# Optimization experiments

Hardware: AMD Instinct MI355X
Metric: run time of the kernel (lower is better)

The kernel has to match this reference:

```python
import jax, jax.numpy as jnp
import numpy as np

DIM = 1024
NUM_HEADS = 16
HEAD_DIM = DIM // NUM_HEADS


def setup_inputs() -> dict:
    key = jax.random.key(0)
    k1, k2, k3, k4, k5 = jax.random.split(key, 5)
    B, N, C = 4, 4096, DIM
    s = 1.0 / np.sqrt(C)
    return {
        "x": jax.random.normal(k1, (B, N, C), dtype=jnp.float32),
        "W_qkv": jax.random.uniform(k2, (C, 3 * C), dtype=jnp.float32, minval=-s, maxval=s),
        "b_qkv": jax.random.uniform(k3, (3 * C,), dtype=jnp.float32, minval=-s, maxval=s),
        "W_proj": jax.random.uniform(k4, (C, C), dtype=jnp.float32, minval=-s, maxval=s),
        "b_proj": jax.random.uniform(k5, (C,), dtype=jnp.float32, minval=-s, maxval=s),
    }


def reference(x, W_qkv, b_qkv, W_proj, b_proj):
    B, N, C = x.shape
    H, D = NUM_HEADS, HEAD_DIM
    qkv = x @ W_qkv + b_qkv                      # [B,N,3C]
    qkv = qkv.reshape(B, N, 3, H, D).transpose(2, 0, 3, 1, 4)  # [3,B,H,N,D]
    q, k, v = qkv[0], qkv[1], qkv[2]
    q = jax.nn.softmax(q, axis=-1)               # softmax over head_dim
    k = jax.nn.softmax(k, axis=-2)               # softmax over sequence N
    context = jnp.einsum('bhnd,bhne->bhde', k, v)  # [B,H,D,D]
    out = jnp.einsum('bhnd,bhde->bhne', q, context)  # [B,H,N,D]
    out = out.transpose(0, 2, 1, 3).reshape(B, N, C)
    return out @ W_proj + b_proj
```

## Files before the change

### kernel.cpp

```cpp
#include <hip/hip_runtime.h>

#define BBATCH 4
#define SEQ 4096
#define CC 1024
#define HH 16
#define DD 64
#define TOKENS 16384
#define QKV3 3072

typedef __attribute__((ext_vector_type(8))) short short8;
typedef __attribute__((ext_vector_type(4))) float floatx4;

__device__ __forceinline__ unsigned short f2bf(float x) {
    unsigned int u = __float_as_uint(x);
    u += 0x7fff + ((u >> 16) & 1);
    return (unsigned short)(u >> 16);
}
__device__ __forceinline__ float bf2f(unsigned short h) {
    return __uint_as_float((unsigned int)h << 16);
}

__device__ __forceinline__ void gload_lds16(const void* g, void* l) {
    __builtin_amdgcn_global_load_lds(
        (const __attribute__((address_space(1))) unsigned int*)g,
        (__attribute__((address_space(3))) unsigned int*)l, 16, 0, 0);
}

__global__ __launch_bounds__(256) void cvt_bf16_kernel(
    const float* __restrict__ X, unsigned short* __restrict__ Y, long n4)
{
    long i = (long)blockIdx.x * 256 + threadIdx.x;
    if (i >= n4) return;
    float4 v = *reinterpret_cast<const float4*>(&X[i * 4]);
    ushort4 h;
    h.x = f2bf(v.x); h.y = f2bf(v.y); h.z = f2bf(v.z); h.w = f2bf(v.w);
    *reinterpret_cast<ushort4*>(&Y[i * 4]) = h;
}

__global__ __launch_bounds__(256) void transpose_bf16_kernel(
    const float* __restrict__ W, int K, int N, unsigned short* __restrict__ T)
{
    __shared__ unsigned short Lh[32][36];
    const int k0 = blockIdx.y * 32, n0 = blockIdx.x * 32;
    const int t = threadIdx.x;
    const int r = t >> 3, c4 = (t & 7) * 4;

    float4 w = *reinterpret_cast<const float4*>(&W[(size_t)(k0 + r) * N + n0 + c4]);
    Lh[r][c4 + 0] = f2bf(w.x);
    Lh[r][c4 + 1] = f2bf(w.y);
    Lh[r][c4 + 2] = f2bf(w.z);
    Lh[r][c4 + 3] = f2bf(w.w);
    __syncthreads();

    const int rn = t >> 3, ck = (t & 7) * 4;
    ushort4 h4;
    h4.x = Lh[ck + 0][rn]; h4.y = Lh[ck + 1][rn];
    h4.z = Lh[ck + 2][rn]; h4.w = Lh[ck + 3][rn];
    *reinterpret_cast<ushort4*>(&T[(size_t)(n0 + rn) * K + k0 + ck]) = h4;
}

template <int MODE>
__global__ __launch_bounds__(512) void gemm256_bf16_kernel(
    const unsigned short* __restrict__ A, int lda,
    const unsigned short* __restrict__ Bt, int ldb,
    const float* __restrict__ bias,
    float* __restrict__ Cf, int ldc,
    unsigned short* __restrict__ Qo, unsigned short* __restrict__ Ko,
    unsigned short* __restrict__ Vo)
{
    __shared__ unsigned short smem[65536];

    const int t = threadIdx.x;
    const int wave = t >> 6, lane = t & 63;

    const int gx = gridDim.x;
    const int nwg = gx * gridDim.y;
    const int id0 = blockIdx.y * gx + blockIdx.x;
    const int cpx = nwg >> 3;
    const int swzid = (id0 & 7) * cpx + (id0 >> 3);
    const int bx = swzid % gx, by = swzid / gx;

    const int row0 = by * 256, col0 = bx * 256;
    const int wave_m = wave >> 2, wave_n = wave & 3;

    const unsigned short* Bp = Bt;
    if (MODE == 0) Bp += ((size_t)(row0 >> 12)) << 20;

    const int fr  = lane & 15;
    const int fqb = (lane >> 4) << 4;
    const int sm  = (fr & 7) << 4;
    const int ck0 = ((0  + fqb) ^ sm) >> 1;
    const int ck1 = ((64 + fqb) ^ sm) >> 1;
    const int aRow = (wave_m * 128 + fr) * 64;
    const int bRow = (wave_n * 64 + fr) * 64;

    int srow[2], scol[2];
#pragma unroll
    for (int e = 0; e < 2; e++) {
        const int P  = (wave << 10) + (lane << 4) + (e << 13);
        const int r  = P >> 7;
        const int pc = P & 127;
        srow[e] = r;
        scol[e] = (pc ^ ((r & 7) << 4)) >> 1;
    }

    auto STAGE_PART = [&](int kt, int buf, int part) {
        const int isB = part >> 1, half = part & 1;
        const unsigned short* p = isB ? Bp : A;
        const int r0 = isB ? col0 : row0;
        const int ld = isB ? ldb : lda;
        const int ldsOff = buf * 32768 + isB * 16384 + half * 8192 + wave * 512;
#pragma unroll
        for (int e = 0; e < 2; e++)
            gload_lds16(&p[(size_t)(r0 + half * 128 + srow[e]) * ld
                           + ((kt & 15) << 6) + scol[e]],
                        &smem[ldsOff + e * 4096]);
    };

    floatx4 acc[8][4];
#pragma unroll
    for (int i = 0; i < 8; i++)
#pragma unroll
        for (int j = 0; j < 4; j++) acc[i][j] = (floatx4)0.0f;

    short8 a[4][2], bl[2][2], bh[2][2];

#define RDA(BUF, IH)                                                          \
    _Pragma("unroll") for (int ii = 0; ii < 4; ii++) {                        \
        a[ii][0] = *reinterpret_cast<const short8*>(                          \
            &smem[(BUF) * 32768 + aRow + ((IH) * 64 + ii * 16) * 64 + ck0]);  \
        a[ii][1] = *reinterpret_cast<const short8*>(                          \
            &smem[(BUF) * 32768 + aRow + ((IH) * 64 + ii * 16) * 64 + ck1]);  \
    }
#define RDB(BUF, JH, DST)                                                     \
    _Pragma("unroll") for (int jj = 0; jj < 2; jj++) {                        \
        DST[jj][0] = *reinterpret_cast<const short8*>(                        \
            &smem[(BUF) * 32768 + 16384 + bRow + ((JH) * 32 + jj * 16) * 64 + ck0]); \
        DST[jj][1] = *reinterpret_cast<const short8*>(                        \
            &smem[(BUF) * 32768 + 16384 + bRow + ((JH) * 32 + jj * 16) * 64 + ck1]); \
    }
#define MFMA_Q(IH, JH, BB)                                                    \
    __builtin_amdgcn_s_setprio(1);                                            \
    _Pragma("unroll") for (int ii = 0; ii < 4; ii++)                          \
    _Pragma("unroll") for (int jj = 0; jj < 2; jj++) {                        \
        acc[(IH)*4+ii][(JH)*2+jj] = __builtin_amdgcn_mfma_f32_16x16x32_bf16(  \
            a[ii][0], BB[jj][0], acc[(IH)*4+ii][(JH)*2+jj], 0, 0, 0);         \
        acc[(IH)*4+ii][(JH)*2+jj] = __builtin_amdgcn_mfma_f32_16x16x32_bf16(  \
            a[ii][1], BB[jj][1], acc[(IH)*4+ii][(JH)*2+jj], 0, 0, 0);         \
    }                                                                         \
    __builtin_amdgcn_s_setprio(0);
#define BARRIER __builtin_amdgcn_s_barrier()
#define WAIT_LGKM asm volatile("s_waitcnt lgkmcnt(0)" ::: "memory")
#define WAIT_VM8  asm volatile("s_waitcnt vmcnt(8)" ::: "memory")

#define KTILE(CUR, TS)                                                        \
    {                                                                         \
        RDA(CUR, 0); RDB(CUR, 0, bl);                                         \
        BARRIER; WAIT_LGKM; MFMA_Q(0, 0, bl); BARRIER;                        \
        RDB(CUR, 1, bh);                                                      \
        BARRIER; WAIT_LGKM; MFMA_Q(0, 1, bh); BARRIER;                        \
        RDA(CUR, 1);                                                          \
        STAGE_PART(TS, CUR, 2); STAGE_PART(TS, CUR, 3);                       \
        BARRIER; WAIT_LGKM; MFMA_Q(1, 1, bh); BARRIER;                        \
        STAGE_PART(TS, CUR, 0); STAGE_PART(TS, CUR, 1);                       \
        WAIT_VM8;                                                             \
        BARRIER;                                                              \
        MFMA_Q(1, 0, bl);                                                     \
        BARRIER;                                                              \
    }

    STAGE_PART(0, 0, 0); STAGE_PART(0, 0, 1);
    STAGE_PART(0, 0, 2); STAGE_PART(0, 0, 3);
    STAGE_PART(1, 1, 0); STAGE_PART(1, 1, 1);
    STAGE_PART(1, 1, 2); STAGE_PART(1, 1, 3);
    WAIT_VM8;
    BARRIER;

#pragma unroll 1
    for (int it = 0; it < 8; it++) {
        KTILE(0, (2 * it + 2) & 15);
        KTILE(1, (2 * it + 3) & 15);
    }

#undef KTILE
#undef WAIT_VM8
#undef WAIT_LGKM
#undef BARRIER
#undef MFMA_Q
#undef RDB
#undef RDA

    const int cn = lane & 15, cq = (lane >> 4) * 4;

    if (MODE == 0) {
#pragma unroll
        for (int j = 0; j < 4; j++) {
            const int col = col0 + wave_n * 64 + j * 16 + cn;
            const float bv = bias[col];
#pragma unroll
            for (int i = 0; i < 8; i++)
#pragma unroll
                for (int r = 0; r < 4; r++) {
                    const int row = row0 + wave_m * 128 + i * 16 + cq + r;
                    Cf[(size_t)row * ldc + col] = acc[i][j][r] + bv;
                }
        }
        return;
    }

    __syncthreads();

#pragma unroll
    for (int j = 0; j < 4; j++) {
        const int colL = wave_n * 64 + j * 16 + cn;
        const float bv = bias[col0 + colL];
#pragma unroll
        for (int i = 0; i < 8; i++)
#pragma unroll
            for (int r = 0; r < 4; r++) {
                const int lr = wave_m * 128 + i * 16 + cq + r;
                smem[lr * 256 + (colL ^ ((lr & 7) << 3))] = f2bf(acc[i][j][r] + bv);
            }
    }
    __syncthreads();

    {
        unsigned short* outp = (bx < 4) ? Qo : ((bx < 8) ? Ko : Vo);
        const bool isQ = (bx < 4);
        const int R = t >> 1, half = t & 1;
        const size_t obase = (size_t)(row0 + R) * CC + (col0 & 1023) + half * 128;
        unsigned short* orow = &outp[obase];

#pragma unroll
        for (int g = 0; g < 2; g++) {
            short8 bufv[8];
            const int cbase = half * 16 + g * 8;
#pragma unroll
            for (int k = 0; k < 8; k++)
                bufv[k] = *reinterpret_cast<const short8*>(
                    &smem[R * 256 + (((cbase + k) ^ (R & 7)) << 3)]);
            if (isQ) {
                float v[64];
                float mx = -3.0e38f;
#pragma unroll
                for (int k = 0; k < 8; k++)
#pragma unroll
                    for (int e = 0; e < 8; e++) {
                        const float f = bf2f((unsigned short)bufv[k][e]);
                        v[k * 8 + e] = f;
                        mx = fmaxf(mx, f);
                    }
                float s = 0.0f;
#pragma unroll
                for (int q = 0; q < 64; q++) {
                    const float ev = __expf(v[q] - mx);
                    v[q] = ev;
                    s += ev;
                }
                const float inv = 1.0f / s;
#pragma unroll
                for (int k = 0; k < 8; k++)
#pragma unroll
                    for (int e = 0; e < 8; e++)
                        bufv[k][e] = (short)f2bf(v[k * 8 + e] * inv);
            }
#pragma unroll
            for (int k = 0; k < 8; k++)
                *reinterpret_cast<short8*>(&orow[g * 64 + k * 8]) = bufv[k];
        }
    }
}

__global__ __launch_bounds__(256) void kv_ctx_kernel(
    const unsigned short* __restrict__ Km, const unsigned short* __restrict__ Vm,
    float* __restrict__ ctx, float* __restrict__ csum)
{
    const int bh = blockIdx.x, ch = blockIdx.y;
    const int b = bh >> 4, h = bh & 15;
    const int t = threadIdx.x;

    __shared__ float Ks[32][68];
    __shared__ float Vs[32][68];
    __shared__ float cred[4][64];

    const int d0 = (t >> 4) * 4, e0 = (t & 15) * 4;
    float acc[4][4];
#pragma unroll
    for (int i = 0; i < 4; i++)
#pragma unroll
        for (int j = 0; j < 4; j++) acc[i][j] = 0.0f;
    float csacc = 0.0f;
    const int dc = t & 63, rq = (t >> 6) * 8;

    const size_t base = (size_t)(b * SEQ + ch * 256) * CC + (size_t)h * 64;

    for (int n0 = 0; n0 < 256; n0 += 32) {
        __syncthreads();
#pragma unroll
        for (int l = 0; l < 2; l++) {
            const int idx = t + l * 256;
            const int r = idx >> 4, c4 = (idx & 15) * 4;
            ushort4 kv = *reinterpret_cast<const ushort4*>(&Km[base + (size_t)(n0 + r) * CC + c4]);
            ushort4 vv = *reinterpret_cast<const ushort4*>(&Vm[base + (size_t)(n0 + r) * CC + c4]);
            float4 kf;
            kf.x = __expf(bf2f(kv.x));
            kf.y = __expf(bf2f(kv.y));
            kf.z = __expf(bf2f(kv.z));
            kf.w = __expf(bf2f(kv.w));
            float4 vf = {bf2f(vv.x), bf2f(vv.y), bf2f(vv.z), bf2f(vv.w)};
            *reinterpret_cast<float4*>(&Ks[r][c4]) = kf;
            *reinterpret_cast<float4*>(&Vs[r][c4]) = vf;
        }
        __syncthreads();

#pragma unroll
        for (int r = 0; r < 8; r++) csacc += Ks[rq + r][dc];

#pragma unroll 8
        for (int n = 0; n < 32; n++) {
            float4 a = *reinterpret_cast<const float4*>(&Ks[n][d0]);
            float4 v4 = *reinterpret_cast<const float4*>(&Vs[n][e0]);
            float a4[4] = {a.x, a.y, a.z, a.w};
            float b4[4] = {v4.x, v4.y, v4.z, v4.w};
#pragma unroll
            for (int i = 0; i < 4; i++)
#pragma unroll
                for (int j = 0; j < 4; j++)
                    acc[i][j] += a4[i] * b4[j];
        }
    }

    __syncthreads();
    cred[t >> 6][dc] = csacc;
    __syncthreads();
    if (t < 64)
        atomicAdd(&csum[(size_t)bh * 64 + t],
                  cred[0][t] + cred[1][t] + cred[2][t] + cred[3][t]);

#pragma unroll
    for (int i = 0; i < 4; i++)
#pragma unroll
        for (int j = 0; j < 4; j++)
            atomicAdd(&ctx[((size_t)bh * 64 + d0 + i) * 64 + e0 + j], acc[i][j]);
}

__global__ __launch_bounds__(256) void weff_kernel(
    const float* __restrict__ ctx, const float* __restrict__ csum,
    const float* __restrict__ Wp, unsigned short* __restrict__ WeffT)
{
    const int bh = blockIdx.x, nc = blockIdx.y;
    const int b = bh >> 4, h = bh & 15;
    const int t = threadIdx.x;

    __shared__ float ctxs[64 * 64];
    __shared__ float cinvs[64];
#pragma unroll
    for (int l = 0; l < 16; l++)
        ctxs[t + l * 256] = ctx[(size_t)bh * 4096 + t + l * 256];
    if (t < 64) cinvs[t] = 1.0f / csum[(size_t)bh * 64 + t];
    __syncthreads();

    const int n = nc * 128 + (t & 127);
    const int dg = (t >> 7) * 32;

    float acc[32];
#pragma unroll
    for (int d = 0; d < 32; d++) acc[d] = 0.0f;

    for (int e = 0; e < 64; e++) {
        const float w = Wp[(size_t)(h * 64 + e) * CC + n];
#pragma unroll
        for (int d = 0; d < 32; d++)
            acc[d] += ctxs[(dg + d) * 64 + e] * w;
    }

    const size_t obase = ((size_t)b << 20) + (size_t)n * CC + h * 64 + dg;
#pragma unroll
    for (int d = 0; d < 32; d += 2) {
        ushort2 o;
        o.x = f2bf(acc[d] * cinvs[dg + d]);
        o.y = f2bf(acc[d + 1] * cinvs[dg + d + 1]);
        *reinterpret_cast<ushort2*>(&WeffT[obase + d]) = o;
    }
}

extern "C" void kernel_launch(void* const* d_in, const int* in_sizes, int n_in,
                              void* d_out, int out_size, void* d_ws, size_t ws_size,
                              hipStream_t stream)
{
    const float* x      = (const float*)d_in[0];
    const float* W_qkv  = (const float*)d_in[1];
    const float* b_qkv  = (const float*)d_in[2];
    const float* W_proj = (const float*)d_in[3];
    const float* b_proj = (const float*)d_in[4];
    float* out = (float*)d_out;

    unsigned short* Qm  = (unsigned short*)d_ws;
    unsigned short* Km  = Qm + (size_t)TOKENS * CC;
    unsigned short* Vm  = Km + (size_t)TOKENS * CC;
    unsigned short* xb  = Vm + (size_t)TOKENS * CC;
    unsigned short* wqT = xb + (size_t)TOKENS * CC;
    unsigned short* WeffT = wqT + (size_t)QKV3 * CC;
    float* ctx  = (float*)(WeffT + (size_t)BBATCH * CC * CC);
    float* csum = ctx + (size_t)64 * 64 * 64;

    hipMemsetAsync(ctx, 0, ((size_t)64 * 64 * 64 + 64 * 64) * sizeof(float), stream);

    cvt_bf16_kernel<<<(TOKENS * CC / 4 + 255) / 256, 256, 0, stream>>>(
        x, xb, (long)TOKENS * CC / 4);
    transpose_bf16_kernel<<<dim3(QKV3 / 32, CC / 32), 256, 0, stream>>>(
        W_qkv, CC, QKV3, wqT);

    gemm256_bf16_kernel<1><<<dim3(QKV3 / 256, TOKENS / 256), 512, 0, stream>>>(
        xb, CC, wqT, CC, b_qkv, (float*)nullptr, 0, Qm, Km, Vm);

    kv_ctx_kernel<<<dim3(BBATCH * HH, 16), 256, 0, stream>>>(Km, Vm, ctx, csum);

    weff_kernel<<<dim3(BBATCH * HH, 8), 256, 0, stream>>>(ctx, csum, W_proj, WeffT);

    gemm256_bf16_kernel<0><<<dim3(CC / 256, TOKENS / 256), 512, 0, stream>>>(
        Qm, CC, WeffT, CC, b_proj, out, CC, nullptr, nullptr, nullptr);
}
```

Baseline: 413.2 us.

## Deepen GEMM K-tile prefetch interleaving and replace ctx atomics with partial-sum reduction

The GEMM main loop now spreads the staging of the next K-tile's quarters across the MFMA phases of the current tile and waits with vmcnt(2) instead of vmcnt(8). This lets global-to-LDS loads overlap compute more evenly. The kv_ctx kernel no longer issues float atomicAdds. It writes per-chunk partial context and column sums into the reused xb workspace, and a new reduce kernel sums them. This removes the memset and atomic contention, at the cost of an extra launch and about 16 MB of partial traffic.

```diff
diff --git a/kernel.cpp b/kernel.cpp
--- a/kernel.cpp
+++ b/kernel.cpp
@@ -151,19 +151,21 @@
     __builtin_amdgcn_s_setprio(0);
 #define BARRIER __builtin_amdgcn_s_barrier()
 #define WAIT_LGKM asm volatile("s_waitcnt lgkmcnt(0)" ::: "memory")
-#define WAIT_VM8  asm volatile("s_waitcnt vmcnt(8)" ::: "memory")
-
-#define KTILE(CUR, TS)                                                        \
+#define WAIT_VM2  asm volatile("s_waitcnt vmcnt(2)" ::: "memory")
+
+#define KTILE(CUR, OTH, TN, TX)                                               \
     {                                                                         \
         RDA(CUR, 0); RDB(CUR, 0, bl);                                         \
+        STAGE_PART(TN, OTH, 1);                                               \
         BARRIER; WAIT_LGKM; MFMA_Q(0, 0, bl); BARRIER;                        \
         RDB(CUR, 1, bh);                                                      \
+        STAGE_PART(TN, OTH, 2);                                               \
         BARRIER; WAIT_LGKM; MFMA_Q(0, 1, bh); BARRIER;                        \
         RDA(CUR, 1);                                                          \
-        STAGE_PART(TS, CUR, 2); STAGE_PART(TS, CUR, 3);                       \
+        STAGE_PART(TN, OTH, 3);                                               \
         BARRIER; WAIT_LGKM; MFMA_Q(1, 1, bh); BARRIER;                        \
-        STAGE_PART(TS, CUR, 0); STAGE_PART(TS, CUR, 1);                       \
-        WAIT_VM8;                                                             \
+        STAGE_PART(TX, CUR, 0);                                               \
+        WAIT_VM2;                                                             \
         BARRIER;                                                              \
         MFMA_Q(1, 0, bl);                                                     \
         BARRIER;                                                              \
@@ -171,19 +173,19 @@
 
     STAGE_PART(0, 0, 0); STAGE_PART(0, 0, 1);
     STAGE_PART(0, 0, 2); STAGE_PART(0, 0, 3);
-    STAGE_PART(1, 1, 0); STAGE_PART(1, 1, 1);
-    STAGE_PART(1, 1, 2); STAGE_PART(1, 1, 3);
-    WAIT_VM8;
+    STAGE_PART(1, 1, 0);
+    WAIT_VM2;
     BARRIER;
 
 #pragma unroll 1
     for (int it = 0; it < 8; it++) {
-        KTILE(0, (2 * it + 2) & 15);
-        KTILE(1, (2 * it + 3) & 15);
+        const int t1 = 2 * it + 1, t2 = 2 * it + 2, t3 = 2 * it + 3;
+        KTILE(0, 1, t1, t2);
+        KTILE(1, 0, t2, t3);
     }
 
 #undef KTILE
-#undef WAIT_VM8
+#undef WAIT_VM2
 #undef WAIT_LGKM
 #undef BARRIER
 #undef MFMA_Q
@@ -273,7 +275,7 @@
 
 __global__ __launch_bounds__(256) void kv_ctx_kernel(
     const unsigned short* __restrict__ Km, const unsigned short* __restrict__ Vm,
-    float* __restrict__ ctx, float* __restrict__ csum)
+    float* __restrict__ ctx_p, float* __restrict__ csum_p)
 {
     const int bh = blockIdx.x, ch = blockIdx.y;
     const int b = bh >> 4, h = bh & 15;
@@ -333,15 +335,42 @@
     __syncthreads();
     cred[t >> 6][dc] = csacc;
     __syncthreads();
+
+    const size_t pslot = (size_t)ch * 64 + bh;
     if (t < 64)
-        atomicAdd(&csum[(size_t)bh * 64 + t],
-                  cred[0][t] + cred[1][t] + cred[2][t] + cred[3][t]);
-
-#pragma unroll
-    for (int i = 0; i < 4; i++)
-#pragma unroll
-        for (int j = 0; j < 4; j++)
-            atomicAdd(&ctx[((size_t)bh * 64 + d0 + i) * 64 + e0 + j], acc[i][j]);
+        csum_p[pslot * 64 + t] =
+            cred[0][t] + cred[1][t] + cred[2][t] + cred[3][t];
+
+    float* cp = &ctx_p[pslot * 4096];
+#pragma unroll
+    for (int i = 0; i < 4; i++) {
+        float4 v4 = {acc[i][0], acc[i][1], acc[i][2], acc[i][3]};
+        *reinterpret_cast<float4*>(&cp[(d0 + i) * 64 + e0]) = v4;
+    }
+}
+
+__global__ __launch_bounds__(256) void reduce_ctx_kernel(
+    const float* __restrict__ ctx_p, const float* __restrict__ csum_p,
+    float* __restrict__ ctx, float* __restrict__ csum)
+{
+    const int bh = blockIdx.x, q = blockIdx.y;
+    const int t = threadIdx.x;
+#pragma unroll
+    for (int e = 0; e < 4; e++) {
+        const int idx = (q * 4 + e) * 256 + t;
+        float s = 0.0f;
+#pragma unroll
+        for (int p = 0; p < 16; p++)
+            s += ctx_p[((size_t)p * 64 + bh) * 4096 + idx];
+        ctx[(size_t)bh * 4096 + idx] = s;
+    }
+    if (q == 0 && t < 64) {
+        float s = 0.0f;
+#pragma unroll
+        for (int p = 0; p < 16; p++)
+            s += csum_p[((size_t)p * 64 + bh) * 64 + t];
+        csum[(size_t)bh * 64 + t] = s;
+    }
 }
 
 __global__ __launch_bounds__(256) void weff_kernel(
@@ -401,10 +430,10 @@
     unsigned short* xb  = Vm + (size_t)TOKENS * CC;
     unsigned short* wqT = xb + (size_t)TOKENS * CC;
     unsigned short* WeffT = wqT + (size_t)QKV3 * CC;
-    float* ctx  = (float*)(WeffT + (size_t)BBATCH * CC * CC);
-    float* csum = ctx + (size_t)64 * 64 * 64;
-
-    hipMemsetAsync(ctx, 0, ((size_t)64 * 64 * 64 + 64 * 64) * sizeof(float), stream);
+    float* ctx    = (float*)(WeffT + (size_t)BBATCH * CC * CC);
+    float* csum   = ctx + (size_t)64 * 4096;
+    float* ctx_p  = (float*)xb;
+    float* csum_p = ctx_p + (size_t)16 * 64 * 4096;
 
     cvt_bf16_kernel<<<(TOKENS * CC / 4 + 255) / 256, 256, 0, stream>>>(
         x, xb, (long)TOKENS * CC / 4);
@@ -414,7 +443,10 @@
     gemm256_bf16_kernel<1><<<dim3(QKV3 / 256, TOKENS / 256), 512, 0, stream>>>(
         xb, CC, wqT, CC, b_qkv, (float*)nullptr, 0, Qm, Km, Vm);
 
-    kv_ctx_kernel<<<dim3(BBATCH * HH, 16), 256, 0, stream>>>(Km, Vm, ctx, csum);
+    kv_ctx_kernel<<<dim3(BBATCH * HH, 16), 256, 0, stream>>>(Km, Vm, ctx_p, csum_p);
+
+    reduce_ctx_kernel<<<dim3(BBATCH * HH, 4), 256, 0, stream>>>(
+        ctx_p, csum_p, ctx, csum);
 
     weff_kernel<<<dim3(BBATCH * HH, 8), 256, 0, stream>>>(ctx, csum, W_proj, WeffT);
 
```

New measurement: 371.3 us. 10.1% less time.
